# Kernel tuning notes

Hardware: AMD Instinct MI355X
Metric: run time of the kernel (lower is better)

## Reference

```python
import jax, jax.numpy as jnp
import numpy as np

EMB = 1024
HEAD = 64
B = 4
S = 4096


def setup_inputs() -> dict:
    key = jax.random.key(0)
    ks = jax.random.split(key, 7)
    std = 1.0 / np.sqrt(EMB)
    return {
        "x": jax.random.normal(ks[0], (B, S, EMB), dtype=jnp.float32),
        "Wq": jax.random.uniform(ks[1], (EMB, HEAD), jnp.float32, -std, std),
        "bq": jax.random.uniform(ks[2], (HEAD,), jnp.float32, -std, std),
        "Wk": jax.random.uniform(ks[3], (EMB, HEAD), jnp.float32, -std, std),
        "bk": jax.random.uniform(ks[4], (HEAD,), jnp.float32, -std, std),
        "Wv": jax.random.uniform(ks[5], (EMB, HEAD), jnp.float32, -std, std),
        "bv": jax.random.uniform(ks[6], (HEAD,), jnp.float32, -std, std),
    }


def reference(x, Wq, bq, Wk, bk, Wv, bv):
    # Q, K, V: [B, S, HEAD]
    Q = x @ Wq + bq
    K = x @ Wk + bk
    V = x @ Wv + bv
    scale = 1.0 / jnp.sqrt(jnp.asarray(HEAD, dtype=Q.dtype))
    # scores: [B, S, S]
    scores = jnp.einsum("bqd,bkd->bqk", Q, K) * scale
    seq = x.shape[1]
    # original mask = tril(randn) sliced; masked_fill where mask==0 => causal
    causal = jnp.tril(jnp.ones((seq, seq), dtype=bool))
    scores = jnp.where(causal, scores, -jnp.inf)
    attn = jax.nn.softmax(scores, axis=-1)
    return jnp.einsum("bqk,bkd->bqd", attn, V)
```

## Files before the change

### kernel.cpp

```cpp
#include <hip/hip_runtime.h>
#include <stdint.h>

#define S_LEN 4096
#define EMB   1024
#define HEAD  64

typedef short bf16x8 __attribute__((ext_vector_type(8)));
typedef float f32x4  __attribute__((ext_vector_type(4)));
typedef float f32x16 __attribute__((ext_vector_type(16)));

#define QSCALE 0.18033688011112042f

__device__ __forceinline__ unsigned short f2bf(float f) {
    union { float f; uint32_t u; } v; v.f = f;
    uint32_t r = v.u + 0x7fffu + ((v.u >> 16) & 1u);
    return (unsigned short)(r >> 16);
}

__device__ __forceinline__ int cvtpk_bf16(float lo, float hi_) {
    int r;
    asm("v_cvt_pk_bf16_f32 %0, %1, %2" : "=v"(r) : "v"(lo), "v"(hi_));
    return r;
}

__global__ void wprep_kernel(const float* __restrict__ Wq,
                             const float* __restrict__ Wk,
                             const float* __restrict__ Wv,
                             unsigned short* __restrict__ wt) {
    __shared__ float t[64][65];
    const int tid = threadIdx.x;
    const int m   = blockIdx.x >> 4;
    const int k0  = (blockIdx.x & 15) << 6;
    const float* W = (m == 0) ? Wq : (m == 1) ? Wk : Wv;
    for (int i = 0; i < 4; ++i) {
        const int k  = (tid >> 4) + i * 16;
        const int n4 = (tid & 15) << 2;
        float4 v = *(const float4*)&W[(k0 + k) * 64 + n4];
        t[k][n4 + 0] = v.x; t[k][n4 + 1] = v.y;
        t[k][n4 + 2] = v.z; t[k][n4 + 3] = v.w;
    }
    __syncthreads();
    const int n = tid >> 2, kq = (tid & 3) << 4;
    __align__(16) unsigned short u[16];
    for (int i = 0; i < 16; ++i) u[i] = f2bf(t[kq + i][n]);
    *(int4*)&wt[(m * 64 + n) * 1024 + k0 + kq]     = *(int4*)&u[0];
    *(int4*)&wt[(m * 64 + n) * 1024 + k0 + kq + 8] = *(int4*)&u[8];
}

__global__ __launch_bounds__(512, 2) void qkv_kernel(
    const float* __restrict__ x, const unsigned short* __restrict__ wt,
    const float* __restrict__ bq, const float* __restrict__ bk,
    const float* __restrict__ bv,
    unsigned short* __restrict__ Qp, unsigned short* __restrict__ Kp,
    unsigned short* __restrict__ Vt) {

    __shared__ __align__(16) unsigned short xs[2][32 * 72];
    __shared__ __align__(16) unsigned short ws[2][192 * 72];

    const int tid  = threadIdx.x;
    const int lane = tid & 63;
    const int w    = tid >> 6;
    const int wm   = w & 1;
    const int wn   = w >> 1;
    const int quad = lane >> 4;
    const int lid  = lane & 15;
    const int row0 = blockIdx.x * 32;

    f32x4 acc[3];
    for (int j = 0; j < 3; ++j) acc[j] = (f32x4){0.f, 0.f, 0.f, 0.f};

#define STAGE(BUF, K0)                                                         \
    do {                                                                       \
        {           \
            int r = tid >> 4, c4 = (tid & 15) << 2;                            \
            float4 v = *(const float4*)&x[(row0 + r) * EMB + (K0) + c4];       \
            ushort4 u;                                                         \
            u.x = f2bf(v.x); u.y = f2bf(v.y); u.z = f2bf(v.z); u.w = f2bf(v.w);\
            *(ushort4*)&xs[BUF][r * 72 + c4] = u;                              \
        }                                                                      \
        for (int i = 0; i < 3; ++i) {      \
            int f = tid + i * 512;                                             \
            int n = f >> 3, kq = (f & 7) << 3;                                 \
            *(int4*)&ws[BUF][n * 72 + kq] =                                    \
                *(const int4*)&wt[(n << 10) + (K0) + kq];                      \
        }                                                                      \
    } while (0)

    STAGE(0, 0);
    __syncthreads();

    for (int kc = 0; kc < 16; ++kc) {
        const int cur = kc & 1;
        if (kc + 1 < 16) STAGE(cur ^ 1, (kc + 1) * 64);
        for (int kk = 0; kk < 2; ++kk) {
            bf16x8 a = *(const bf16x8*)&xs[cur][(wm * 16 + lid) * 72 + kk * 32 + quad * 8];
            for (int nt = 0; nt < 3; ++nt) {
                bf16x8 bfr = *(const bf16x8*)&ws[cur][(wn * 48 + nt * 16 + lid) * 72 + kk * 32 + quad * 8];
                acc[nt] = __builtin_amdgcn_mfma_f32_16x16x32_bf16(a, bfr, acc[nt], 0, 0, 0);
            }
        }
        __syncthreads();
    }
#undef STAGE

    for (int nt = 0; nt < 3; ++nt) {
        const int col = wn * 48 + nt * 16 + lid;
        const int mid = col >> 6;
        const int lc  = col & 63;
        const float bias = (mid == 0) ? bq[lc] : (mid == 1) ? bk[lc] : bv[lc];
        const int rb = row0 + wm * 16 + quad * 4;
        f32x4 v = acc[nt];
        if (mid == 0) {
            for (int j = 0; j < 4; ++j)
                Qp[(rb + j) * 64 + lc] = f2bf((v[j] + bias) * QSCALE);
        } else if (mid == 1) {
            for (int j = 0; j < 4; ++j)
                Kp[(rb + j) * 64 + lc] = f2bf(v[j] + bias);
        } else {
            const int bb = rb >> 12, s = rb & 4095;
            ushort4 u;
            u.x = f2bf(v[0] + bias); u.y = f2bf(v[1] + bias);
            u.z = f2bf(v[2] + bias); u.w = f2bf(v[3] + bias);
            *(ushort4*)&Vt[(bb * 64 + lc) * S_LEN + s] = u;
        }
    }
}

__global__ __launch_bounds__(512, 2) void flash_kernel(
    const unsigned short* __restrict__ Qp, const unsigned short* __restrict__ Kp,
    const unsigned short* __restrict__ Vt, float* __restrict__ out) {

    __shared__ __align__(16) float Obuf[8][32][66];
    __shared__ float lbuf[8][32];

    const int tid  = threadIdx.x;
    const int lane = tid & 63;
    const int w    = tid >> 6;
    const int hi   = lane >> 5;
    const int l5   = lane & 31;

    const int l  = blockIdx.x;
    const int x  = l & 7;
    const int m  = l >> 3;
    const int j  = m & 31;
    const int r  = m >> 5;
    const int b  = x & 3;
    const int h  = x >> 2;
    const int qt = (h == 0) ? (r ? j : 127 - j)
                            : (r ? 32 + j : 95 - j);
    const int q0 = qt * 32;
    const int nt = qt + 1;

    bf16x8 qf[4];
#pragma unroll
    for (int dk = 0; dk < 4; ++dk)
        qf[dk] = *(const bf16x8*)&Qp[(b * S_LEN + q0 + l5) * 64 + dk * 16 + hi * 8];

    f32x16 O0 = {}, O1 = {};
    float ls = 0.f;

    const unsigned short* Kb = &Kp[b * S_LEN * 64];
    const unsigned short* Vb = &Vt[b * 64 * S_LEN];

    int t = w;
    bf16x8 kf[4];
    if (t < nt) {
#pragma unroll
        for (int dk = 0; dk < 4; ++dk)
            kf[dk] = *(const bf16x8*)&Kb[(t * 32 + l5) * 64 + dk * 16 + hi * 8];
    }

    while (t < nt) {
        const int kt = t << 5;
        bf16x8 vf[2][2];
#pragma unroll
        for (int dh = 0; dh < 2; ++dh)
#pragma unroll
            for (int kc = 0; kc < 2; ++kc)
                vf[dh][kc] = *(const bf16x8*)&Vb[(dh * 32 + l5) * S_LEN + kt + kc * 16 + hi * 8];

        __builtin_amdgcn_s_setprio(1);
        f32x16 st = {};
#pragma unroll
        for (int dk = 0; dk < 4; ++dk)
            st = __builtin_amdgcn_mfma_f32_32x32x16_bf16(kf[dk], qf[dk], st, 0, 0, 0);
        __builtin_amdgcn_s_setprio(0);

        const int tn = t + 8;
        if (tn < nt) {
#pragma unroll
            for (int dk = 0; dk < 4; ++dk)
                kf[dk] = *(const bf16x8*)&Kb[(tn * 32 + l5) * 64 + dk * 16 + hi * 8];
        }

        if (t == nt - 1) {
#pragma unroll
            for (int rr = 0; rr < 16; ++rr) {
                const int key = kt + (rr & 3) + 8 * (rr >> 2) + 4 * hi;
                if (key > q0 + l5) st[rr] = -1e30f;
            }
        }

#pragma unroll
        for (int kc = 0; kc < 2; ++kc) {
            const int c8 = kc * 8;
            float ev[8];
#pragma unroll
            for (int i = 0; i < 8; ++i) ev[i] = exp2f(st[c8 + i]);
            ls += ((ev[0] + ev[1]) + (ev[2] + ev[3])) +
                  ((ev[4] + ev[5]) + (ev[6] + ev[7]));
            const int p0 = cvtpk_bf16(ev[0], ev[1]);
            const int p1 = cvtpk_bf16(ev[2], ev[3]);
            const int p2 = cvtpk_bf16(ev[4], ev[5]);
            const int p3 = cvtpk_bf16(ev[6], ev[7]);
            auto s02 = __builtin_amdgcn_permlane32_swap(p0, p2, false, false);
            auto s13 = __builtin_amdgcn_permlane32_swap(p1, p3, false, false);
            union { int wd[4]; bf16x8 v; } pf;
            pf.wd[0] = s02[0]; pf.wd[1] = s13[0];
            pf.wd[2] = s02[1]; pf.wd[3] = s13[1];
            __builtin_amdgcn_s_setprio(1);
            O0 = __builtin_amdgcn_mfma_f32_32x32x16_bf16(pf.v, vf[0][kc], O0, 0, 0, 0);
            O1 = __builtin_amdgcn_mfma_f32_32x32x16_bf16(pf.v, vf[1][kc], O1, 0, 0, 0);
            __builtin_amdgcn_s_setprio(0);
        }
        t = tn;
    }

    const float lt = ls + __shfl_xor(ls, 32);
#pragma unroll
    for (int rr = 0; rr < 16; ++rr) {
        const int row = (rr & 3) + 8 * (rr >> 2) + 4 * hi;
        Obuf[w][row][l5]      = O0[rr];
        Obuf[w][row][32 + l5] = O1[rr];
    }
    if (lane < 32) lbuf[w][l5] = lt;
    __syncthreads();

    const int col = tid & 63;
    const int r0  = tid >> 6;
    for (int ii = 0; ii < 4; ++ii) {
        const int row = r0 + ii * 8;
        float o = 0.f, lsum = 0.f;
        for (int ww = 0; ww < 8; ++ww) {
            o    += Obuf[ww][row][col];
            lsum += lbuf[ww][row];
        }
        out[(b * S_LEN + q0 + row) * 64 + col] = o / lsum;
    }
}

extern "C" void kernel_launch(void* const* d_in, const int* in_sizes, int n_in,
                              void* d_out, int out_size, void* d_ws, size_t ws_size,
                              hipStream_t stream) {
    const float* x  = (const float*)d_in[0];
    const float* Wq = (const float*)d_in[1];
    const float* bq = (const float*)d_in[2];
    const float* Wk = (const float*)d_in[3];
    const float* bk = (const float*)d_in[4];
    const float* Wv = (const float*)d_in[5];
    const float* bv = (const float*)d_in[6];
    float* out = (float*)d_out;

    unsigned short* wt = (unsigned short*)d_ws;
    unsigned short* Qp = wt + 196608;
    unsigned short* Kp = Qp + 1048576;
    unsigned short* Vt = Kp + 1048576;

    hipLaunchKernelGGL(wprep_kernel, dim3(48), dim3(256), 0, stream, Wq, Wk, Wv, wt);
    hipLaunchKernelGGL(qkv_kernel, dim3(512), dim3(512), 0, stream,
                       x, wt, bq, bk, bv, Qp, Kp, Vt);
    hipLaunchKernelGGL(flash_kernel, dim3(512), dim3(512), 0, stream,
                       Qp, Kp, Vt, out);
}
```

Baseline: 154.7 us.

## Double QKV row tile, stage swizzled weights via direct global-to-LDS loads

The QKV projection now processes 64 rows per block instead of 32, so each staged weight chunk is reused across twice as many rows and the grid is halved. The weight prep kernel writes a chunk-major, XOR-swizzled layout that qkv_kernel copies straight into LDS with global_load_lds, which drops the register round-trip and the padding. The flash kernel swaps exp2f for the raw hardware exp2 builtin. The larger tile means fewer blocks to fill the GPU and more accumulators per wave.

```diff
diff --git a/kernel.cpp b/kernel.cpp
--- a/kernel.cpp
+++ b/kernel.cpp
@@ -8,6 +8,7 @@
 typedef short bf16x8 __attribute__((ext_vector_type(8)));
 typedef float f32x4  __attribute__((ext_vector_type(4)));
 typedef float f32x16 __attribute__((ext_vector_type(16)));
+typedef unsigned short ushort8 __attribute__((ext_vector_type(8)));
 
 #define QSCALE 0.18033688011112042f
 
@@ -21,6 +22,12 @@
     int r;
     asm("v_cvt_pk_bf16_f32 %0, %1, %2" : "=v"(r) : "v"(lo), "v"(hi_));
     return r;
+}
+
+__device__ __forceinline__ void gload_lds16(const void* g, void* l) {
+    __builtin_amdgcn_global_load_lds(
+        (const __attribute__((address_space(1))) void*)g,
+        (__attribute__((address_space(3))) void*)l, 16, 0, 0);
 }
 
 __global__ void wprep_kernel(const float* __restrict__ Wq,
@@ -30,7 +37,8 @@
     __shared__ float t[64][65];
     const int tid = threadIdx.x;
     const int m   = blockIdx.x >> 4;
-    const int k0  = (blockIdx.x & 15) << 6;
+    const int kcb = blockIdx.x & 15;
+    const int k0  = kcb << 6;
     const float* W = (m == 0) ? Wq : (m == 1) ? Wk : Wv;
     for (int i = 0; i < 4; ++i) {
         const int k  = (tid >> 4) + i * 16;
@@ -43,8 +51,12 @@
     const int n = tid >> 2, kq = (tid & 3) << 4;
     __align__(16) unsigned short u[16];
     for (int i = 0; i < 16; ++i) u[i] = f2bf(t[kq + i][n]);
-    *(int4*)&wt[(m * 64 + n) * 1024 + k0 + kq]     = *(int4*)&u[0];
-    *(int4*)&wt[(m * 64 + n) * 1024 + k0 + kq + 8] = *(int4*)&u[8];
+    const int nimg = m * 64 + n;
+    const int base = kcb * 12288 + nimg * 64;
+    const int c0   = (kq >> 3) ^ (n & 7);
+    const int c1   = ((kq >> 3) + 1) ^ (n & 7);
+    *(int4*)&wt[base + c0 * 8] = *(int4*)&u[0];
+    *(int4*)&wt[base + c1 * 8] = *(int4*)&u[8];
 }
 
 __global__ __launch_bounds__(512, 2) void qkv_kernel(
@@ -54,35 +66,40 @@
     unsigned short* __restrict__ Qp, unsigned short* __restrict__ Kp,
     unsigned short* __restrict__ Vt) {
 
-    __shared__ __align__(16) unsigned short xs[2][32 * 72];
-    __shared__ __align__(16) unsigned short ws[2][192 * 72];
+    __shared__ __align__(16) unsigned short xs[2][64 * 72];
+    __shared__ __align__(16) unsigned short ws[2][12288];
 
     const int tid  = threadIdx.x;
     const int lane = tid & 63;
     const int w    = tid >> 6;
-    const int wm   = w & 1;
-    const int wn   = w >> 1;
+    const int wm   = w & 3;
+    const int wn   = w >> 2;
     const int quad = lane >> 4;
     const int lid  = lane & 15;
-    const int row0 = blockIdx.x * 32;
-
-    f32x4 acc[3];
-    for (int j = 0; j < 3; ++j) acc[j] = (f32x4){0.f, 0.f, 0.f, 0.f};
-
-#define STAGE(BUF, K0)                                                         \
+    const int row0 = blockIdx.x * 64;
+
+    f32x4 acc[6];
+    for (int j = 0; j < 6; ++j) acc[j] = (f32x4){0.f, 0.f, 0.f, 0.f};
+
+#define STAGE(BUF, KC)                                                         \
     do {                                                                       \
-        {           \
-            int r = tid >> 4, c4 = (tid & 15) << 2;                            \
-            float4 v = *(const float4*)&x[(row0 + r) * EMB + (K0) + c4];       \
-            ushort4 u;                                                         \
-            u.x = f2bf(v.x); u.y = f2bf(v.y); u.z = f2bf(v.z); u.w = f2bf(v.w);\
-            *(ushort4*)&xs[BUF][r * 72 + c4] = u;                              \
+        {             \
+            int rr = tid >> 3, c8 = (tid & 7) << 3;                            \
+            const float* xp = &x[(row0 + rr) * EMB + (KC) * 64 + c8];          \
+            float4 v0 = *(const float4*)xp;                                    \
+            float4 v1 = *(const float4*)(xp + 4);                              \
+            ushort8 u;                                                         \
+            u[0] = f2bf(v0.x); u[1] = f2bf(v0.y);                              \
+            u[2] = f2bf(v0.z); u[3] = f2bf(v0.w);                              \
+            u[4] = f2bf(v1.x); u[5] = f2bf(v1.y);                              \
+            u[6] = f2bf(v1.z); u[7] = f2bf(v1.w);                              \
+            *(ushort8*)&xs[BUF][rr * 72 + c8] = u;                             \
         }                                                                      \
-        for (int i = 0; i < 3; ++i) {      \
-            int f = tid + i * 512;                                             \
-            int n = f >> 3, kq = (f & 7) << 3;                                 \
-            *(int4*)&ws[BUF][n * 72 + kq] =                                    \
-                *(const int4*)&wt[(n << 10) + (K0) + kq];                      \
+        {          \
+            const unsigned short* gs = &wt[(KC) * 12288 + w * 1536 + lane * 8];\
+            gload_lds16(gs,        &ws[BUF][w * 1536]);                        \
+            gload_lds16(gs +  512, &ws[BUF][w * 1536 +  512]);                 \
+            gload_lds16(gs + 1024, &ws[BUF][w * 1536 + 1024]);                 \
         }                                                                      \
     } while (0)
 
@@ -91,11 +108,13 @@
 
     for (int kc = 0; kc < 16; ++kc) {
         const int cur = kc & 1;
-        if (kc + 1 < 16) STAGE(cur ^ 1, (kc + 1) * 64);
+        if (kc + 1 < 16) STAGE(cur ^ 1, kc + 1);
         for (int kk = 0; kk < 2; ++kk) {
             bf16x8 a = *(const bf16x8*)&xs[cur][(wm * 16 + lid) * 72 + kk * 32 + quad * 8];
-            for (int nt = 0; nt < 3; ++nt) {
-                bf16x8 bfr = *(const bf16x8*)&ws[cur][(wn * 48 + nt * 16 + lid) * 72 + kk * 32 + quad * 8];
+            const int swz = ((((kk << 2) | quad) ^ (lid & 7)) << 3);
+            for (int nt = 0; nt < 6; ++nt) {
+                const int n = wn * 96 + nt * 16 + lid;
+                bf16x8 bfr = *(const bf16x8*)&ws[cur][n * 64 + swz];
                 acc[nt] = __builtin_amdgcn_mfma_f32_16x16x32_bf16(a, bfr, acc[nt], 0, 0, 0);
             }
         }
@@ -103,8 +122,8 @@
     }
 #undef STAGE
 
-    for (int nt = 0; nt < 3; ++nt) {
-        const int col = wn * 48 + nt * 16 + lid;
+    for (int nt = 0; nt < 6; ++nt) {
+        const int col = wn * 96 + nt * 16 + lid;
         const int mid = col >> 6;
         const int lc  = col & 63;
         const float bias = (mid == 0) ? bq[lc] : (mid == 1) ? bk[lc] : bv[lc];
@@ -206,7 +225,7 @@
             const int c8 = kc * 8;
             float ev[8];
 #pragma unroll
-            for (int i = 0; i < 8; ++i) ev[i] = exp2f(st[c8 + i]);
+            for (int i = 0; i < 8; ++i) ev[i] = __builtin_amdgcn_exp2f(st[c8 + i]);
             ls += ((ev[0] + ev[1]) + (ev[2] + ev[3])) +
                   ((ev[4] + ev[5]) + (ev[6] + ev[7]));
             const int p0 = cvtpk_bf16(ev[0], ev[1]);
@@ -267,7 +286,7 @@
     unsigned short* Vt = Kp + 1048576;
 
     hipLaunchKernelGGL(wprep_kernel, dim3(48), dim3(256), 0, stream, Wq, Wk, Wv, wt);
-    hipLaunchKernelGGL(qkv_kernel, dim3(512), dim3(512), 0, stream,
+    hipLaunchKernelGGL(qkv_kernel, dim3(256), dim3(512), 0, stream,
                        x, wt, bq, bk, bv, Qp, Kp, Vt);
     hipLaunchKernelGGL(flash_kernel, dim3(512), dim3(512), 0, stream,
                        Qp, Kp, Vt, out);
```

Result: no change. 153.2 us (-1.0%).
